# Kernel optimization log

Hardware: AMD Instinct MI355X
Metric: run time of the kernel (lower is better)

## Reference

```python
import jax, jax.numpy as jnp
import numpy as np

N_NODES = 50000
N_EDGES = 800000
EMB_DIM = 128
HID = 256


def setup_inputs() -> dict:
    key = jax.random.key(0)
    ks = jax.random.split(key, 9)
    src = jax.random.randint(ks[0], (N_EDGES,), 0, N_NODES, dtype=jnp.int32)
    dst = jax.random.randint(ks[1], (N_EDGES,), 0, N_NODES, dtype=jnp.int32)
    emb = jax.random.normal(ks[2], (N_NODES, EMB_DIM), dtype=jnp.float32)
    s1 = 1.0 / np.sqrt(EMB_DIM)
    s2 = 1.0 / np.sqrt(HID)
    W1 = jax.random.uniform(ks[3], (EMB_DIM, HID), jnp.float32, -s1, s1)
    b1 = jax.random.uniform(ks[4], (HID,), jnp.float32, -s1, s1)
    W2 = jax.random.uniform(ks[5], (HID, HID), jnp.float32, -s2, s2)
    b2 = jax.random.uniform(ks[6], (HID,), jnp.float32, -s2, s2)
    W3 = jax.random.uniform(ks[7], (HID, EMB_DIM), jnp.float32, -s2, s2)
    b3 = jax.random.uniform(ks[8], (EMB_DIM,), jnp.float32, -s2, s2)
    return {"src": src, "dst": dst, "emb": emb,
            "W1": W1, "b1": b1, "W2": W2, "b2": b2, "W3": W3, "b3": b3}


def _gin_conv(x, src, dst, W, b):
    # DGL GINConv 'max': (1+eps)*h + max over in-neighbors; eps=0 default.
    agg = jax.ops.segment_max(x[src], dst, num_segments=N_NODES)  # [N, d]
    agg = jnp.where(agg == -jnp.inf, 0.0, agg)  # isolated nodes -> 0 (DGL fill)
    return (x + agg) @ W + b


def reference(src, dst, emb, W1, b1, W2, b2, W3, b3):
    x = _gin_conv(emb, src, dst, W1, b1)
    x = jax.nn.relu(x)
    x = _gin_conv(x, src, dst, W2, b2)
    x = jax.nn.relu(x)
    out = _gin_conv(x, src, dst, W3, b3)  # no relu on last layer
    return out
```

## Files before the change

kernel.cpp:

```cpp
#include <hip/hip_runtime.h>
#include <math.h>

#define EMB 128
#define HIDN 256

typedef _Float16 half8 __attribute__((ext_vector_type(8)));
typedef _Float16 half4 __attribute__((ext_vector_type(4)));
typedef float f32x4 __attribute__((ext_vector_type(4)));
typedef unsigned short u16;


__global__ void hist_kernel(const int* __restrict__ dst, int E, int* __restrict__ cnt) {
    int i = blockIdx.x * blockDim.x + threadIdx.x;
    if (i < E) atomicAdd(&cnt[dst[i]], 1);
}

__global__ void scan_partial(const int* __restrict__ cnt, int* __restrict__ partials, int Nn) {
    __shared__ int red[256];
    const int b = blockIdx.x, t = threadIdx.x;
    const int base = b * 1024 + t * 4;
    int s = 0;
#pragma unroll
    for (int i = 0; i < 4; ++i)
        if (base + i < Nn) s += cnt[base + i];
    red[t] = s;
    __syncthreads();
    for (int d = 128; d > 0; d >>= 1) {
        if (t < d) red[t] += red[t + d];
        __syncthreads();
    }
    if (t == 0) partials[b] = red[0];
}

__global__ void scan_top(int* __restrict__ partials, int nB) {
    __shared__ int s[256];
    const int t = threadIdx.x;
    int orig = (t < nB) ? partials[t] : 0;
    s[t] = orig;
    __syncthreads();
    for (int d = 1; d < 256; d <<= 1) {
        int v = (t >= d) ? s[t - d] : 0;
        __syncthreads();
        s[t] += v;
        __syncthreads();
    }
    if (t < nB) partials[t] = s[t] - orig;
}

__global__ void scan_apply(const int* __restrict__ cnt, const int* __restrict__ pbase,
                           int* __restrict__ off, int* __restrict__ cur, int Nn, int E) {
    __shared__ int tsum[256];
    const int b = blockIdx.x, t = threadIdx.x;
    const int base = b * 1024 + t * 4;
    int c[4];
#pragma unroll
    for (int i = 0; i < 4; ++i) c[i] = (base + i < Nn) ? cnt[base + i] : 0;
    int s = c[0] + c[1] + c[2] + c[3];
    tsum[t] = s;
    __syncthreads();
    for (int d = 1; d < 256; d <<= 1) {
        int v = (t >= d) ? tsum[t - d] : 0;
        __syncthreads();
        tsum[t] += v;
        __syncthreads();
    }
    int run = pbase[b] + ((t == 0) ? 0 : tsum[t - 1]);
#pragma unroll
    for (int i = 0; i < 4; ++i) {
        int idx = base + i;
        if (idx < Nn) {
            off[idx] = run;
            cur[idx] = run;
            run += c[i];
        }
    }
    if (b == 0 && t == 0) off[Nn] = E;
}

__global__ void scatter_kernel(const int* __restrict__ src, const int* __restrict__ dst,
                               int E, int* __restrict__ cur, u16* __restrict__ sorted) {
    int i = blockIdx.x * blockDim.x + threadIdx.x;
    if (i < E) {
        int d = dst[i];
        int p = atomicAdd(&cur[d], 1);
        sorted[p] = (u16)src[i];
    }
}


__device__ __forceinline__ void pack_w_one(const float* __restrict__ W, _Float16* __restrict__ Wg,
                                           int K, int N, int i) {
    if (i < (K / 8) * N) {
        int j = i / N, n = i - j * N;
        half8 h;
#pragma unroll
        for (int q = 0; q < 8; ++q) h[q] = (_Float16)W[(size_t)(j * 8 + q) * N + n];
        *reinterpret_cast<half8*>(Wg + (size_t)i * 8) = h;
    }
}

__global__ void prep_kernel(int* __restrict__ cur, int Nn,
                            const float* __restrict__ emb, _Float16* __restrict__ buf0, int n4,
                            const float* __restrict__ W1, _Float16* __restrict__ Wg1,
                            const float* __restrict__ W2, _Float16* __restrict__ Wg2,
                            const float* __restrict__ W3, _Float16* __restrict__ Wg3,
                            int bZeroEnd, int bCvtEnd, int bW1End, int bW2End, int bW3End) {
    const int b = blockIdx.x;
    const int t = threadIdx.x;
    if (b < bZeroEnd) {
        int i = b * 256 + t;
        if (i < Nn) cur[i] = 0;
    } else if (b < bCvtEnd) {
        int i = (b - bZeroEnd) * 256 + t;
        if (i < n4) {
            float4 v = *reinterpret_cast<const float4*>(emb + (size_t)i * 4);
            half4 h;
            h[0] = (_Float16)v.x; h[1] = (_Float16)v.y;
            h[2] = (_Float16)v.z; h[3] = (_Float16)v.w;
            *reinterpret_cast<half4*>(buf0 + (size_t)i * 4) = h;
        }
    } else if (b < bW1End) {
        pack_w_one(W1, Wg1, EMB, HIDN, (b - bCvtEnd) * 256 + t);
    } else if (b < bW2End) {
        pack_w_one(W2, Wg2, HIDN, HIDN, (b - bW1End) * 256 + t);
    } else if (b < bW3End) {
        pack_w_one(W3, Wg3, HIDN, EMB, (b - bW2End) * 256 + t);
    }
}


template <int K>
__global__ __launch_bounds__(256) void segmax_g(
    const _Float16* __restrict__ x, const int* __restrict__ off,
    const u16* __restrict__ sorted, _Float16* __restrict__ xg, int Nn)
{
    constexpr int NG = 512 / K;
    constexpr int LPR = 64 / NG;
    const int node = blockIdx.x * 4 + (threadIdx.x >> 6);
    const int lane = threadIdx.x & 63;
    if (node >= Nn) return;
    const int g = lane / LPR;
    const int colh = (lane % LPR) * 8;
    const int beg = off[node];
    const int end = off[node + 1];
    const _Float16* xcol = x + colh;

    half8 acc;
#pragma unroll
    for (int i = 0; i < 8; ++i) acc[i] = (_Float16)(-INFINITY);

#pragma unroll 4
    for (int e = beg + g; e < end; e += NG) {
        int s = (int)sorted[e];
        half8 v = *reinterpret_cast<const half8*>(xcol + (size_t)s * K);
        acc = __builtin_elementwise_max(acc, v);
    }

    union U { half8 h; int i[4]; };
    if (NG == 4) {
        U a, b; a.h = acc;
#pragma unroll
        for (int k = 0; k < 4; ++k) b.i[k] = __shfl_xor(a.i[k], 16);
        acc = __builtin_elementwise_max(a.h, b.h);
    }
    {
        U a, b; a.h = acc;
#pragma unroll
        for (int k = 0; k < 4; ++k) b.i[k] = __shfl_xor(a.i[k], 32);
        acc = __builtin_elementwise_max(a.h, b.h);
    }

    if (g == 0) {
        const bool hasEdges = (end > beg);
        half8 xv = *reinterpret_cast<const half8*>(x + (size_t)node * K + colh);
        half8 o;
#pragma unroll
        for (int i = 0; i < 8; ++i)
            o[i] = (_Float16)((float)xv[i] + (hasEdges ? (float)acc[i] : 0.0f));
        const int j = lane;
        size_t gidx = ((size_t)(node >> 6) * (K / 8) + j) * 64 + (node & 63);
        *reinterpret_cast<half8*>(xg + gidx * 8) = o;
    }
}


template <int K, int N, int RB, int CB, int OUT_F32, int RELU>
__global__ __launch_bounds__(256) void gemm_g(
    const _Float16* __restrict__ xg, const _Float16* __restrict__ Wg,
    const float* __restrict__ bias, void* __restrict__ C, int Nn)
{
    const int wave = threadIdx.x >> 6;
    const int lane = threadIdx.x & 63;
    const int wr = wave / CB, wc = wave % CB;
    const int rowTile = blockIdx.x * RB + wr;
    const int node0 = rowTile * 64;
    const int r  = lane & 15;
    const int gq = lane >> 4;
    const int cb = wc * 64;

    f32x4 acc[4][4];
#pragma unroll
    for (int mi = 0; mi < 4; ++mi)
#pragma unroll
        for (int ni = 0; ni < 4; ++ni) acc[mi][ni] = (f32x4){0.f, 0.f, 0.f, 0.f};

    const _Float16* Ab = xg + (size_t)rowTile * K * 64;

    for (int k0 = 0; k0 < K; k0 += 32) {
        const int jb = (k0 >> 3) + gq;
        half8 aF[4], bF[4];
#pragma unroll
        for (int mi = 0; mi < 4; ++mi)
            aF[mi] = *reinterpret_cast<const half8*>(Ab + (size_t)((jb << 6) + mi * 16 + r) * 8);
#pragma unroll
        for (int ni = 0; ni < 4; ++ni)
            bF[ni] = *reinterpret_cast<const half8*>(Wg + ((size_t)jb * N + cb + ni * 16 + r) * 8);
#pragma unroll
        for (int mi = 0; mi < 4; ++mi)
#pragma unroll
            for (int ni = 0; ni < 4; ++ni)
                acc[mi][ni] = __builtin_amdgcn_mfma_f32_16x16x32_f16(aF[mi], bF[ni], acc[mi][ni], 0, 0, 0);
    }

#pragma unroll
    for (int ni = 0; ni < 4; ++ni) {
        int colC = cb + ni * 16 + r;
        float bv = bias[colC];
#pragma unroll
        for (int mi = 0; mi < 4; ++mi) {
#pragma unroll
            for (int q = 0; q < 4; ++q) {
                int row = node0 + mi * 16 + (gq << 2) + q;
                if (row < Nn) {
                    float v = acc[mi][ni][q] + bv;
                    if (RELU) v = fmaxf(v, 0.f);
                    if (OUT_F32) ((float*)C)[(size_t)row * N + colC] = v;
                    else         ((_Float16*)C)[(size_t)row * N + colC] = (_Float16)v;
                }
            }
        }
    }
}


extern "C" void kernel_launch(void* const* d_in, const int* in_sizes, int n_in,
                              void* d_out, int out_size, void* d_ws, size_t ws_size,
                              hipStream_t stream) {
    const int*   src = (const int*)d_in[0];
    const int*   dst = (const int*)d_in[1];
    const float* emb = (const float*)d_in[2];
    const float* W1  = (const float*)d_in[3];
    const float* b1  = (const float*)d_in[4];
    const float* W2  = (const float*)d_in[5];
    const float* b2  = (const float*)d_in[6];
    const float* W3  = (const float*)d_in[7];
    const float* b3  = (const float*)d_in[8];
    float* out = (float*)d_out;

    const int E  = in_sizes[0];
    const int Nn = in_sizes[2] / EMB;
    const int nTiles = (Nn + 63) / 64;

    char* ws = (char*)d_ws;
    auto align256 = [](size_t x) { return (x + 255) & ~(size_t)255; };
    size_t p = 0;
    int* off      = (int*)(ws + p); p = align256(p + (size_t)(Nn + 1) * 4);
    int* cur      = (int*)(ws + p); p = align256(p + (size_t)(Nn + 1) * 4);
    int* partials = (int*)(ws + p); p = align256(p + 256 * 4);
    u16* sorted   = (u16*)(ws + p); p = align256(p + (size_t)E * 2);
    _Float16* buf0 = (_Float16*)(ws + p); p = align256(p + (size_t)Nn * HIDN * 2);
    _Float16* buf1 = (_Float16*)(ws + p); p = align256(p + (size_t)Nn * HIDN * 2);
    _Float16* xg   = (_Float16*)(ws + p); p = align256(p + (size_t)(nTiles + 2) * 64 * HIDN * 2);
    _Float16* Wg1  = (_Float16*)(ws + p); p = align256(p + (size_t)EMB * HIDN * 2);
    _Float16* Wg2  = (_Float16*)(ws + p); p = align256(p + (size_t)HIDN * HIDN * 2);
    _Float16* Wg3  = (_Float16*)(ws + p); p = align256(p + (size_t)HIDN * EMB * 2);

    const int n4 = Nn * EMB / 4;
    const int bZeroEnd = (Nn + 255) / 256;
    const int bCvtEnd  = bZeroEnd + (n4 + 255) / 256;
    const int bW1End   = bCvtEnd + (EMB / 8 * HIDN + 255) / 256;
    const int bW2End   = bW1End + (HIDN / 8 * HIDN + 255) / 256;
    const int bW3End   = bW2End + (HIDN / 8 * EMB + 255) / 256;
    prep_kernel<<<bW3End, 256, 0, stream>>>(cur, Nn, emb, buf0, n4,
                                            W1, Wg1, W2, Wg2, W3, Wg3,
                                            bZeroEnd, bCvtEnd, bW1End, bW2End, bW3End);

    const int nScanBlocks = (Nn + 1023) / 1024;
    hist_kernel<<<(E + 255) / 256, 256, 0, stream>>>(dst, E, cur);
    scan_partial<<<nScanBlocks, 256, 0, stream>>>(cur, partials, Nn);
    scan_top<<<1, 256, 0, stream>>>(partials, nScanBlocks);
    scan_apply<<<nScanBlocks, 256, 0, stream>>>(cur, partials, off, cur, Nn, E);
    scatter_kernel<<<(E + 255) / 256, 256, 0, stream>>>(src, dst, E, cur, sorted);

    const int segBlocks = (Nn + 3) / 4;

    segmax_g<128><<<segBlocks, 256, 0, stream>>>(buf0, off, sorted, xg, Nn);
    gemm_g<128, 256, 1, 4, 0, 1><<<nTiles, 256, 0, stream>>>(xg, Wg1, b1, buf1, Nn);

    segmax_g<256><<<segBlocks, 256, 0, stream>>>(buf1, off, sorted, xg, Nn);
    gemm_g<256, 256, 1, 4, 0, 1><<<nTiles, 256, 0, stream>>>(xg, Wg2, b2, buf0, Nn);

    segmax_g<256><<<segBlocks, 256, 0, stream>>>(buf0, off, sorted, xg, Nn);
    gemm_g<256, 128, 2, 2, 1, 0><<<(nTiles + 1) / 2, 256, 0, stream>>>(xg, Wg3, b3, out, Nn);
}
```

Baseline: 303.9 us.

## Merge histogram into prep kernel, fold scan top into apply, stage segmax stores

Moves the destination histogram into the prep kernel and zeroes the counters with a memset. It drops the single-block scan_top kernel by having each scan_apply block reduce its preceding partials with wave shuffles. The segmax kernel now stages each block's four node outputs in shared memory so the gather-layout writes to xg are coalesced across nodes. It also raises the edge-loop unroll. Fewer launches and better store coalescing are traded for an extra barrier and a memset call, and the prefix reduction assumes at most 64 scan blocks.

```diff
diff --git a/kernel.cpp b/kernel.cpp
--- a/kernel.cpp
+++ b/kernel.cpp
@@ -10,10 +10,46 @@
 typedef unsigned short u16;
 
 
-__global__ void hist_kernel(const int* __restrict__ dst, int E, int* __restrict__ cnt) {
-    int i = blockIdx.x * blockDim.x + threadIdx.x;
-    if (i < E) atomicAdd(&cnt[dst[i]], 1);
-}
+__device__ __forceinline__ void pack_w_one(const float* __restrict__ W, _Float16* __restrict__ Wg,
+                                           int K, int N, int i) {
+    if (i < (K / 8) * N) {
+        int j = i / N, n = i - j * N;
+        half8 h;
+#pragma unroll
+        for (int q = 0; q < 8; ++q) h[q] = (_Float16)W[(size_t)(j * 8 + q) * N + n];
+        *reinterpret_cast<half8*>(Wg + (size_t)i * 8) = h;
+    }
+}
+
+__global__ void prep_kernel(const int* __restrict__ dst, int E, int* __restrict__ cur,
+                            const float* __restrict__ emb, _Float16* __restrict__ buf0, int n4,
+                            const float* __restrict__ W1, _Float16* __restrict__ Wg1,
+                            const float* __restrict__ W2, _Float16* __restrict__ Wg2,
+                            const float* __restrict__ W3, _Float16* __restrict__ Wg3,
+                            int bCvtEnd, int bHistEnd, int bW1End, int bW2End, int bW3End) {
+    const int b = blockIdx.x;
+    const int t = threadIdx.x;
+    if (b < bCvtEnd) {
+        int i = b * 256 + t;
+        if (i < n4) {
+            float4 v = *reinterpret_cast<const float4*>(emb + (size_t)i * 4);
+            half4 h;
+            h[0] = (_Float16)v.x; h[1] = (_Float16)v.y;
+            h[2] = (_Float16)v.z; h[3] = (_Float16)v.w;
+            *reinterpret_cast<half4*>(buf0 + (size_t)i * 4) = h;
+        }
+    } else if (b < bHistEnd) {
+        int i = (b - bCvtEnd) * 256 + t;
+        if (i < E) atomicAdd(&cur[dst[i]], 1);
+    } else if (b < bW1End) {
+        pack_w_one(W1, Wg1, EMB, HIDN, (b - bHistEnd) * 256 + t);
+    } else if (b < bW2End) {
+        pack_w_one(W2, Wg2, HIDN, HIDN, (b - bW1End) * 256 + t);
+    } else if (b < bW3End) {
+        pack_w_one(W3, Wg3, HIDN, EMB, (b - bW2End) * 256 + t);
+    }
+}
+
 
 __global__ void scan_partial(const int* __restrict__ cnt, int* __restrict__ partials, int Nn) {
     __shared__ int red[256];
@@ -32,25 +68,17 @@
     if (t == 0) partials[b] = red[0];
 }
 
-__global__ void scan_top(int* __restrict__ partials, int nB) {
-    __shared__ int s[256];
-    const int t = threadIdx.x;
-    int orig = (t < nB) ? partials[t] : 0;
-    s[t] = orig;
-    __syncthreads();
-    for (int d = 1; d < 256; d <<= 1) {
-        int v = (t >= d) ? s[t - d] : 0;
-        __syncthreads();
-        s[t] += v;
-        __syncthreads();
-    }
-    if (t < nB) partials[t] = s[t] - orig;
-}
-
-__global__ void scan_apply(const int* __restrict__ cnt, const int* __restrict__ pbase,
-                           int* __restrict__ off, int* __restrict__ cur, int Nn, int E) {
+__global__ void scan_apply(const int* __restrict__ cnt, const int* __restrict__ partials,
+                           int nB, int* __restrict__ off, int* __restrict__ cur, int Nn, int E) {
     __shared__ int tsum[256];
+    __shared__ int sbase;
     const int b = blockIdx.x, t = threadIdx.x;
+    if (t < 64) {
+        int v = (t < b && t < nB) ? partials[t] : 0;
+#pragma unroll
+        for (int m = 1; m < 64; m <<= 1) v += __shfl_xor(v, m);
+        if (t == 0) sbase = v;
+    }
     const int base = b * 1024 + t * 4;
     int c[4];
 #pragma unroll
@@ -64,7 +92,7 @@
         tsum[t] += v;
         __syncthreads();
     }
-    int run = pbase[b] + ((t == 0) ? 0 : tsum[t - 1]);
+    int run = sbase + ((t == 0) ? 0 : tsum[t - 1]);
 #pragma unroll
     for (int i = 0; i < 4; ++i) {
         int idx = base + i;
@@ -88,47 +116,6 @@
 }
 
 
-__device__ __forceinline__ void pack_w_one(const float* __restrict__ W, _Float16* __restrict__ Wg,
-                                           int K, int N, int i) {
-    if (i < (K / 8) * N) {
-        int j = i / N, n = i - j * N;
-        half8 h;
-#pragma unroll
-        for (int q = 0; q < 8; ++q) h[q] = (_Float16)W[(size_t)(j * 8 + q) * N + n];
-        *reinterpret_cast<half8*>(Wg + (size_t)i * 8) = h;
-    }
-}
-
-__global__ void prep_kernel(int* __restrict__ cur, int Nn,
-                            const float* __restrict__ emb, _Float16* __restrict__ buf0, int n4,
-                            const float* __restrict__ W1, _Float16* __restrict__ Wg1,
-                            const float* __restrict__ W2, _Float16* __restrict__ Wg2,
-                            const float* __restrict__ W3, _Float16* __restrict__ Wg3,
-                            int bZeroEnd, int bCvtEnd, int bW1End, int bW2End, int bW3End) {
-    const int b = blockIdx.x;
-    const int t = threadIdx.x;
-    if (b < bZeroEnd) {
-        int i = b * 256 + t;
-        if (i < Nn) cur[i] = 0;
-    } else if (b < bCvtEnd) {
-        int i = (b - bZeroEnd) * 256 + t;
-        if (i < n4) {
-            float4 v = *reinterpret_cast<const float4*>(emb + (size_t)i * 4);
-            half4 h;
-            h[0] = (_Float16)v.x; h[1] = (_Float16)v.y;
-            h[2] = (_Float16)v.z; h[3] = (_Float16)v.w;
-            *reinterpret_cast<half4*>(buf0 + (size_t)i * 4) = h;
-        }
-    } else if (b < bW1End) {
-        pack_w_one(W1, Wg1, EMB, HIDN, (b - bCvtEnd) * 256 + t);
-    } else if (b < bW2End) {
-        pack_w_one(W2, Wg2, HIDN, HIDN, (b - bW1End) * 256 + t);
-    } else if (b < bW3End) {
-        pack_w_one(W3, Wg3, HIDN, EMB, (b - bW2End) * 256 + t);
-    }
-}
-
-
 template <int K>
 __global__ __launch_bounds__(256) void segmax_g(
     const _Float16* __restrict__ x, const int* __restrict__ off,
@@ -136,50 +123,66 @@
 {
     constexpr int NG = 512 / K;
     constexpr int LPR = 64 / NG;
-    const int node = blockIdx.x * 4 + (threadIdx.x >> 6);
+    __shared__ _Float16 sm[4][K];
+
+    const int wave = threadIdx.x >> 6;
     const int lane = threadIdx.x & 63;
-    if (node >= Nn) return;
-    const int g = lane / LPR;
-    const int colh = (lane % LPR) * 8;
-    const int beg = off[node];
-    const int end = off[node + 1];
-    const _Float16* xcol = x + colh;
-
-    half8 acc;
-#pragma unroll
-    for (int i = 0; i < 8; ++i) acc[i] = (_Float16)(-INFINITY);
-
-#pragma unroll 4
-    for (int e = beg + g; e < end; e += NG) {
-        int s = (int)sorted[e];
-        half8 v = *reinterpret_cast<const half8*>(xcol + (size_t)s * K);
-        acc = __builtin_elementwise_max(acc, v);
-    }
-
-    union U { half8 h; int i[4]; };
-    if (NG == 4) {
-        U a, b; a.h = acc;
-#pragma unroll
-        for (int k = 0; k < 4; ++k) b.i[k] = __shfl_xor(a.i[k], 16);
-        acc = __builtin_elementwise_max(a.h, b.h);
-    }
-    {
-        U a, b; a.h = acc;
-#pragma unroll
-        for (int k = 0; k < 4; ++k) b.i[k] = __shfl_xor(a.i[k], 32);
-        acc = __builtin_elementwise_max(a.h, b.h);
-    }
-
-    if (g == 0) {
-        const bool hasEdges = (end > beg);
-        half8 xv = *reinterpret_cast<const half8*>(x + (size_t)node * K + colh);
-        half8 o;
-#pragma unroll
-        for (int i = 0; i < 8; ++i)
-            o[i] = (_Float16)((float)xv[i] + (hasEdges ? (float)acc[i] : 0.0f));
-        const int j = lane;
-        size_t gidx = ((size_t)(node >> 6) * (K / 8) + j) * 64 + (node & 63);
-        *reinterpret_cast<half8*>(xg + gidx * 8) = o;
+    const int node0 = blockIdx.x * 4;
+    const int node = node0 + wave;
+
+    if (node < Nn) {
+        const int g = lane / LPR;
+        const int colh = (lane % LPR) * 8;
+        const int beg = off[node];
+        const int end = off[node + 1];
+        const _Float16* xcol = x + colh;
+
+        half8 acc;
+#pragma unroll
+        for (int i = 0; i < 8; ++i) acc[i] = (_Float16)(-INFINITY);
+
+#pragma unroll 8
+        for (int e = beg + g; e < end; e += NG) {
+            int s = (int)sorted[e];
+            half8 v = *reinterpret_cast<const half8*>(xcol + (size_t)s * K);
+            acc = __builtin_elementwise_max(acc, v);
+        }
+
+        union U { half8 h; int i[4]; };
+        if (NG == 4) {
+            U a, b; a.h = acc;
+#pragma unroll
+            for (int k = 0; k < 4; ++k) b.i[k] = __shfl_xor(a.i[k], 16);
+            acc = __builtin_elementwise_max(a.h, b.h);
+        }
+        {
+            U a, b; a.h = acc;
+#pragma unroll
+            for (int k = 0; k < 4; ++k) b.i[k] = __shfl_xor(a.i[k], 32);
+            acc = __builtin_elementwise_max(a.h, b.h);
+        }
+
+        if (g == 0) {
+            const bool hasEdges = (end > beg);
+            half8 xv = *reinterpret_cast<const half8*>(x + (size_t)node * K + colh);
+            half8 o;
+#pragma unroll
+            for (int i = 0; i < 8; ++i)
+                o[i] = (_Float16)((float)xv[i] + (hasEdges ? (float)acc[i] : 0.0f));
+            *reinterpret_cast<half8*>(&sm[wave][colh]) = o;
+        }
+    }
+    __syncthreads();
+
+    const int t = threadIdx.x;
+    if (t < 4 * (K / 8)) {
+        const int j = t >> 2, nd = t & 3;
+        const int node2 = node0 + nd;
+        if (node2 < Nn) {
+            half8 o2 = *reinterpret_cast<half8*>(&sm[nd][j * 8]);
+            size_t gidx = ((size_t)(node2 >> 6) * (K / 8) + j) * 64 + (node2 & 63);
+            *reinterpret_cast<half8*>(xg + gidx * 8) = o2;
+        }
     }
 }
 
@@ -275,21 +278,20 @@
     _Float16* Wg2  = (_Float16*)(ws + p); p = align256(p + (size_t)HIDN * HIDN * 2);
     _Float16* Wg3  = (_Float16*)(ws + p); p = align256(p + (size_t)HIDN * EMB * 2);
 
+    hipMemsetAsync(cur, 0, (size_t)Nn * 4, stream);
     const int n4 = Nn * EMB / 4;
-    const int bZeroEnd = (Nn + 255) / 256;
-    const int bCvtEnd  = bZeroEnd + (n4 + 255) / 256;
-    const int bW1End   = bCvtEnd + (EMB / 8 * HIDN + 255) / 256;
+    const int bCvtEnd  = (n4 + 255) / 256;
+    const int bHistEnd = bCvtEnd + (E + 255) / 256;
+    const int bW1End   = bHistEnd + (EMB / 8 * HIDN + 255) / 256;
     const int bW2End   = bW1End + (HIDN / 8 * HIDN + 255) / 256;
     const int bW3End   = bW2End + (HIDN / 8 * EMB + 255) / 256;
-    prep_kernel<<<bW3End, 256, 0, stream>>>(cur, Nn, emb, buf0, n4,
+    prep_kernel<<<bW3End, 256, 0, stream>>>(dst, E, cur, emb, buf0, n4,
                                             W1, Wg1, W2, Wg2, W3, Wg3,
-                                            bZeroEnd, bCvtEnd, bW1End, bW2End, bW3End);
+                                            bCvtEnd, bHistEnd, bW1End, bW2End, bW3End);
 
     const int nScanBlocks = (Nn + 1023) / 1024;
-    hist_kernel<<<(E + 255) / 256, 256, 0, stream>>>(dst, E, cur);
     scan_partial<<<nScanBlocks, 256, 0, stream>>>(cur, partials, Nn);
-    scan_top<<<1, 256, 0, stream>>>(partials, nScanBlocks);
-    scan_apply<<<nScanBlocks, 256, 0, stream>>>(cur, partials, off, cur, Nn, E);
+    scan_apply<<<nScanBlocks, 256, 0, stream>>>(cur, partials, nScanBlocks, off, cur, Nn, E);
     scatter_kernel<<<(E + 255) / 256, 256, 0, stream>>>(src, dst, E, cur, sorted);
 
     const int segBlocks = (Nn + 3) / 4;
```

Result: no change. 303.3 us (-0.2%).
